# Optimization experiments

Measured on AMD Instinct MI355X. Metric: run time of the kernel, lower is better.

The kernel has to match this reference:

```python
import jax, jax.numpy as jnp
import numpy as np

D_MODEL = 1024
N_HEADS = 16
D_HEAD = D_MODEL // N_HEADS
B, S = 4, 2048


def setup_inputs() -> dict:
    key = jax.random.key(0)
    ks = jax.random.split(key, 12)
    std = 1.0 / np.sqrt(D_MODEL)
    inp = {
        "q": jax.random.normal(ks[0], (B, S, D_MODEL), jnp.float32),
        "k": jax.random.normal(ks[1], (B, S, D_MODEL), jnp.float32),
        "v": jax.random.normal(ks[2], (B, S, D_MODEL), jnp.float32),
        # causal mask: 1 where attention is disallowed (j > i)
        "mask": jnp.triu(jnp.ones((S, S), jnp.int32), k=1)[None, None],
        "Wq": jax.random.normal(ks[3], (D_MODEL, D_MODEL), jnp.float32) * std,
        "bq": jnp.zeros((D_MODEL,), jnp.float32),
        "Wk": jax.random.normal(ks[4], (D_MODEL, D_MODEL), jnp.float32) * std,
        "bk": jnp.zeros((D_MODEL,), jnp.float32),
        "Wv": jax.random.normal(ks[5], (D_MODEL, D_MODEL), jnp.float32) * std,
        "bv": jnp.zeros((D_MODEL,), jnp.float32),
        "Wo": jax.random.normal(ks[6], (D_MODEL, D_MODEL), jnp.float32) * std,
        "bo": jnp.zeros((D_MODEL,), jnp.float32),
    }
    return inp


def _split_heads(x):
    # [B, S, D] -> [B, H, S, d_head]
    b, s, _ = x.shape
    return x.reshape(b, s, N_HEADS, D_HEAD).transpose(0, 2, 1, 3)


def reference(q, k, v, mask, Wq, bq, Wk, bk, Wv, bv, Wo, bo):
    # torch Linear: y = x @ W.T + b
    qh = _split_heads(q @ Wq.T + bq)
    kh = _split_heads(k @ Wk.T + bk)
    vh = _split_heads(v @ Wv.T + bv)
    # NOTE: original scales by sqrt(d_model), not sqrt(d_head)
    scale = 1.0 / np.sqrt(D_MODEL).astype(np.float32)
    logits = jnp.einsum("bhqd,bhkd->bhqk", qh, kh) * scale
    logits = logits + mask.astype(logits.dtype) * (-1e9)
    weights = jax.nn.softmax(logits, axis=-1)
    attn = jnp.einsum("bhqk,bhkd->bhqd", weights, vh)
    attn = attn.transpose(0, 2, 1, 3).reshape(q.shape[0], -1, D_MODEL)
    out = attn @ Wo.T + bo
    return out, weights
```

## Files before the change

### kernel.cpp

```cpp
#include <hip/hip_runtime.h>
#include <stdint.h>

typedef unsigned short u16;
typedef __attribute__((ext_vector_type(8))) short bf16x8;
typedef __attribute__((ext_vector_type(8))) unsigned short us8;
typedef __attribute__((ext_vector_type(4))) float f32x4;

typedef __attribute__((address_space(1))) void as1_void;
typedef __attribute__((address_space(3))) void as3_void;

#define S_LEN 2048
#define DMODEL 1024
#define DH 64
#define NHEADS 16
#define NB 4
#define GM (NB * S_LEN)
#define GN DMODEL
#define GK DMODEL
#define SCALE 0.03125f

__device__ __forceinline__ void gload16(const void* g, void* l) {
  __builtin_amdgcn_global_load_lds((const as1_void*)g, (as3_void*)l, 16, 0, 0);
}
__device__ __forceinline__ float bf2f(u16 u) {
  union { unsigned int i; float f; } x; x.i = ((unsigned int)u) << 16; return x.f;
}
__device__ __forceinline__ u16 f2bf(float f) {
  union { float f; unsigned int i; } x; x.f = f;
  unsigned int u = x.i + 0x7fffu + ((x.i >> 16) & 1u);
  return (u16)(u >> 16);
}
__device__ __forceinline__ f32x4 mfma16(bf16x8 a, bf16x8 b, f32x4 c) {
  return __builtin_amdgcn_mfma_f32_16x16x32_bf16(a, b, c, 0, 0, 0);
}
__device__ __forceinline__ void nt_store4(f32x4 v, float* p) {
  __builtin_nontemporal_store(v, (f32x4*)p);
}

__device__ __forceinline__ void cvt_chunk(const float* s, u16* d, int i) {
  const f32x4 a = *(const f32x4*)(s + (size_t)i * 8);
  const f32x4 b = *(const f32x4*)(s + (size_t)i * 8 + 4);
  us8 o;
  o[0] = f2bf(a[0]); o[1] = f2bf(a[1]); o[2] = f2bf(a[2]); o[3] = f2bf(a[3]);
  o[4] = f2bf(b[0]); o[5] = f2bf(b[1]); o[6] = f2bf(b[2]); o[7] = f2bf(b[3]);
  *(us8*)(d + (size_t)i * 8) = o;
}
__global__ __launch_bounds__(256)
void cvt3(const float* __restrict__ s0, const float* __restrict__ s1,
          const float* __restrict__ s2, u16* __restrict__ d0,
          u16* __restrict__ d1, u16* __restrict__ d2, int n8) {
  const int i = blockIdx.x * 256 + threadIdx.x;
  if (i >= n8) return;
  const float* s; u16* d;
  if (blockIdx.y == 0)      { s = s0; d = d0; }
  else if (blockIdx.y == 1) { s = s1; d = d1; }
  else                      { s = s2; d = d2; }
  cvt_chunk(s, d, i);
}
__global__ __launch_bounds__(256)
void cvt4(const float* __restrict__ s0, const float* __restrict__ s1,
          const float* __restrict__ s2, const float* __restrict__ s3,
          u16* __restrict__ d0, u16* __restrict__ d1,
          u16* __restrict__ d2, u16* __restrict__ d3, int n8) {
  const int i = blockIdx.x * 256 + threadIdx.x;
  if (i >= n8) return;
  const float* s; u16* d;
  if (blockIdx.y == 0)      { s = s0; d = d0; }
  else if (blockIdx.y == 1) { s = s1; d = d1; }
  else if (blockIdx.y == 2) { s = s2; d = d2; }
  else                      { s = s3; d = d3; }
  cvt_chunk(s, d, i);
}

#define GEMM_IDX                                                              \
  const int tid  = threadIdx.x;                                               \
  const int lane = tid & 63;                                                  \
  const int wvi  = tid >> 6;                                                  \
  const int wr   = wvi >> 1, wc = wvi & 1;                                    \
  const int rlow = lane & 15, rhi = lane >> 4;

#define GEMM_COMPUTE(Ab, Bb)                                                  \
  {                                                                           \
    bf16x8 af[4][2], bfr[4][2];                                               \
    _Pragma("unroll")                                                         \
    for (int mi = 0; mi < 4; ++mi) {                                          \
      const int row = wr * 64 + mi * 16 + rlow;                               \
      _Pragma("unroll")                                                       \
      for (int k2 = 0; k2 < 2; ++k2)                                          \
        af[mi][k2] = *(const bf16x8*)&(Ab)[row * 64 +                         \
                     (((rhi + k2 * 4) ^ (row & 7)) << 3)];                    \
    }                                                                         \
    _Pragma("unroll")                                                         \
    for (int ni = 0; ni < 4; ++ni) {                                          \
      const int row = wc * 64 + ni * 16 + rlow;                               \
      _Pragma("unroll")                                                       \
      for (int k2 = 0; k2 < 2; ++k2)                                          \
        bfr[ni][k2] = *(const bf16x8*)&(Bb)[row * 64 +                        \
                      (((rhi + k2 * 4) ^ (row & 7)) << 3)];                   \
    }                                                                         \
    _Pragma("unroll")                                                         \
    for (int mi = 0; mi < 4; ++mi)                                            \
      _Pragma("unroll")                                                       \
      for (int ni = 0; ni < 4; ++ni) {                                        \
        acc[mi][ni] = mfma16(af[mi][0], bfr[ni][0], acc[mi][ni]);             \
        acc[mi][ni] = mfma16(af[mi][1], bfr[ni][1], acc[mi][ni]);             \
      }                                                                       \
  }

__global__ __launch_bounds__(256, 3)
void gemm_qkv(const u16* __restrict__ xq, const u16* __restrict__ xk,
              const u16* __restrict__ xv, const u16* __restrict__ wq,
              const u16* __restrict__ wk, const u16* __restrict__ wv,
              const float* __restrict__ bq, const float* __restrict__ bk,
              const float* __restrict__ bv, u16* __restrict__ oq,
              u16* __restrict__ ok, u16* __restrict__ ov) {
  __shared__ u16 smem[2 * 8192];
  u16* As = smem;
  u16* Bs = smem + 8192;
  const u16 *A, *W; const float* bias; u16* C;
  if (blockIdx.z == 0)      { A = xq; W = wq; bias = bq; C = oq; }
  else if (blockIdx.z == 1) { A = xk; W = wk; bias = bk; C = ok; }
  else                      { A = xv; W = wv; bias = bv; C = ov; }
  GEMM_IDX
  const int m0 = blockIdx.x * 128;
  const int n0 = blockIdx.y * 128;

  f32x4 acc[4][4];
#pragma unroll
  for (int i = 0; i < 4; ++i)
#pragma unroll
    for (int j = 0; j < 4; ++j) acc[i][j] = (f32x4){0.f, 0.f, 0.f, 0.f};

  const int nk = GK >> 6;
  for (int kk = 0; kk < nk; ++kk) {
#pragma unroll
    for (int i = 0; i < 4; ++i) {
      const int c = i * 256 + tid;
      const int row = c >> 3, cw = c & 7;
      const int koff = (kk << 6) + ((cw ^ (row & 7)) << 3);
      gload16(A + (size_t)(m0 + row) * GK + koff, &As[(c - lane) << 3]);
      gload16(W + (size_t)(n0 + row) * GK + koff, &Bs[(c - lane) << 3]);
    }
    __syncthreads();
    GEMM_COMPUTE(As, Bs)
    __syncthreads();
  }

  {
    u16* Cs = smem;
#pragma unroll
    for (int ni = 0; ni < 4; ++ni) {
      const int col = wc * 64 + ni * 16 + rlow;
      const float bv2 = bias[n0 + col];
#pragma unroll
      for (int mi = 0; mi < 4; ++mi)
#pragma unroll
        for (int r = 0; r < 4; ++r)
          Cs[(wr * 64 + mi * 16 + rhi * 4 + r) * 128 + col] = f2bf(acc[mi][ni][r] + bv2);
    }
    __syncthreads();
#pragma unroll
    for (int i = 0; i < 8; ++i) {
      const int c = i * 256 + tid;
      const int row = c >> 4, cw = c & 15;
      const us8 t = *(const us8*)&Cs[row * 128 + cw * 8];
      *(us8*)&C[(size_t)(m0 + row) * GN + n0 + cw * 8] = t;
    }
  }
}

__global__ __launch_bounds__(256, 2)
void gemm_o(const u16* __restrict__ A, const u16* __restrict__ W,
            const float* __restrict__ bias, float* __restrict__ C) {
  __shared__ u16 smem[4 * 8192];
  u16* As = smem;
  u16* Bs = smem + 2 * 8192;
  GEMM_IDX
  const int m0 = blockIdx.x * 128;
  const int n0 = blockIdx.y * 128;

  f32x4 acc[4][4];
#pragma unroll
  for (int i = 0; i < 4; ++i)
#pragma unroll
    for (int j = 0; j < 4; ++j) acc[i][j] = (f32x4){0.f, 0.f, 0.f, 0.f};

#define STAGE_G(bufi, kk)                                                     \
  {                                                                           \
    _Pragma("unroll")                                                         \
    for (int i = 0; i < 4; ++i) {                                             \
      const int c = i * 256 + tid;                                            \
      const int row = c >> 3, cw = c & 7;                                     \
      const int koff = ((kk) << 6) + ((cw ^ (row & 7)) << 3);                 \
      gload16(A + (size_t)(m0 + row) * GK + koff,                             \
              &As[(bufi) * 8192 + ((c - lane) << 3)]);                        \
      gload16(W + (size_t)(n0 + row) * GK + koff,                             \
              &Bs[(bufi) * 8192 + ((c - lane) << 3)]);                        \
    }                                                                         \
  }

  const int nk = GK >> 6;
  STAGE_G(0, 0);
  __syncthreads();
  int buf = 0;
  for (int kk = 0; kk < nk; ++kk) {
    if (kk + 1 < nk) STAGE_G(buf ^ 1, kk + 1);
    const u16* Ab = &As[buf * 8192];
    const u16* Bb = &Bs[buf * 8192];
    GEMM_COMPUTE(Ab, Bb)
    __syncthreads();
    buf ^= 1;
  }
#undef STAGE_G

  {
    float* Cs = (float*)smem;
#pragma unroll
    for (int ni = 0; ni < 4; ++ni) {
      const int col = wc * 64 + ni * 16 + rlow;
      const float bv2 = bias[n0 + col];
#pragma unroll
      for (int mi = 0; mi < 4; ++mi)
#pragma unroll
        for (int r = 0; r < 4; ++r)
          Cs[(wr * 64 + mi * 16 + rhi * 4 + r) * 128 + col] = acc[mi][ni][r] + bv2;
    }
    __syncthreads();
#pragma unroll
    for (int i = 0; i < 16; ++i) {
      const int c = i * 256 + tid;
      const int row = c >> 5, cw = c & 31;
      const f32x4 t = *(const f32x4*)&Cs[row * 128 + cw * 4];
      nt_store4(t, &C[(size_t)(m0 + row) * GN + n0 + cw * 4]);
    }
  }
}

__global__ __launch_bounds__(512, 4)
void attn_fused(const u16* __restrict__ qh, const u16* __restrict__ kh,
                const u16* __restrict__ vh, float* __restrict__ wout,
                u16* __restrict__ am)
{
  __shared__ u16 smem[34304];
  u16* Ws  = smem;
  u16* Qs  = smem;
  u16* Kb1 = smem;
  u16* Kb0 = smem + 17408;
  u16* VT  = smem + 17408 + 8192;

  const int tid = threadIdx.x, lane = tid & 63, wv = tid >> 6;
  const int rlow = lane & 15, rhi = lane >> 4;
  const int idx = blockIdx.x;
  const int bh  = idx & 63;
  const int qt  = 15 - (idx >> 6);
  const int b = bh >> 4, h = bh & 15;
  const int q0 = qt << 7;
  const size_t headoff = (size_t)b * S_LEN * DMODEL + h * DH;

#define STAGE_K(dst, jtile)                                                   \
  {                                                                           \
    _Pragma("unroll")                                                         \
    for (int i = 0; i < 2; ++i) {                                             \
      const int c = i * 512 + tid;                                            \
      const int row = c >> 3, cw = c & 7;                                     \
      gload16(kh + headoff + (size_t)((jtile) * 128 + row) * DMODEL +         \
              ((cw ^ (row & 7)) << 3), &(dst)[(c - lane) << 3]);              \
    }                                                                         \
  }
#define LOAD_V(jtile)                                                         \
  {                                                                           \
    const int d0v = wv << 3;                                                  \
    vvA = *(const bf16x8*)(vh + headoff +                                     \
          (size_t)((jtile) * 128 + lane) * DMODEL + d0v);                     \
    vvB = *(const bf16x8*)(vh + headoff +                                     \
          (size_t)((jtile) * 128 + 64 + lane) * DMODEL + d0v);                \
  }

#pragma unroll
  for (int i = 0; i < 2; ++i) {
    const int c = i * 512 + tid;
    const int row = c >> 3, cw = c & 7;
    gload16(qh + headoff + (size_t)(q0 + row) * DMODEL + ((cw ^ (row & 7)) << 3),
            &Qs[(c - lane) << 3]);
  }
  __syncthreads();
  bf16x8 qf[2];
  {
    const int row = wv * 16 + rlow;
#pragma unroll
    for (int k2 = 0; k2 < 2; ++k2)
      qf[k2] = *(const bf16x8*)&Qs[row * 64 + (((rhi + k2 * 4) ^ (row & 7)) << 3)];
  }

  const int gi_base = q0 + wv * 16 + rhi * 4;
  float ssum[4] = {0.f, 0.f, 0.f, 0.f};

  STAGE_K(Kb0, 0);
  for (int jt = 0; jt <= qt; ++jt) {
    __syncthreads();
    const u16* kcur = (jt & 1) ? Kb1 : Kb0;
    if (jt < qt) {
      u16* knxt = (jt & 1) ? Kb0 : Kb1;
      STAGE_K(knxt, jt + 1);
    }
    const bool diag = (jt == qt);
    float pexp[4] = {0.f, 0.f, 0.f, 0.f};
#pragma unroll
    for (int half = 0; half < 2; ++half) {
      f32x4 acc[4];
#pragma unroll
      for (int ni = 0; ni < 4; ++ni) acc[ni] = (f32x4){0.f, 0.f, 0.f, 0.f};
#pragma unroll
      for (int k2 = 0; k2 < 2; ++k2) {
#pragma unroll
        for (int ni = 0; ni < 4; ++ni) {
          const int row = (half * 4 + ni) * 16 + rlow;
          bf16x8 kf = *(const bf16x8*)&kcur[row * 64 + (((rhi + k2 * 4) ^ (row & 7)) << 3)];
          acc[ni] = mfma16(qf[k2], kf, acc[ni]);
        }
      }
#pragma unroll
      for (int ni = 0; ni < 4; ++ni) {
        const int gj = jt * 128 + (half * 4 + ni) * 16 + rlow;
#pragma unroll
        for (int r = 0; r < 4; ++r) {
          if (!diag || gj <= gi_base + r) pexp[r] += __expf(acc[ni][r] * SCALE);
        }
      }
    }
#pragma unroll
    for (int r = 0; r < 4; ++r) {
      float p = pexp[r];
      p += __shfl_xor(p, 1);
      p += __shfl_xor(p, 2);
      p += __shfl_xor(p, 4);
      p += __shfl_xor(p, 8);
      ssum[r] += p;
    }
  }
  float inv_s[4];
#pragma unroll
  for (int r = 0; r < 4; ++r) inv_s[r] = 1.f / ssum[r];

  f32x4 opv[4];
#pragma unroll
  for (int ni = 0; ni < 4; ++ni) opv[ni] = (f32x4){0.f, 0.f, 0.f, 0.f};

  bf16x8 vvA, vvB;
  __syncthreads();
  STAGE_K(Kb0, 0);
  LOAD_V(0);
  __syncthreads();

  for (int jt = 0; jt <= qt; ++jt) {
    {
      const int d0v = wv << 3;
#pragma unroll
      for (int e = 0; e < 8; ++e) {
        VT[(d0v + e) * 136 + lane] = (u16)vvA[e];
        VT[(d0v + e) * 136 + 64 + lane] = (u16)vvB[e];
      }
    }
    const bool diag = (jt == qt);
#pragma unroll
    for (int half = 0; half < 2; ++half) {
      f32x4 acc[4];
#pragma unroll
      for (int ni = 0; ni < 4; ++ni) acc[ni] = (f32x4){0.f, 0.f, 0.f, 0.f};
#pragma unroll
      for (int k2 = 0; k2 < 2; ++k2) {
#pragma unroll
        for (int ni = 0; ni < 4; ++ni) {
          const int row = (half * 4 + ni) * 16 + rlow;
          bf16x8 kf = *(const bf16x8*)&Kb0[row * 64 + (((rhi + k2 * 4) ^ (row & 7)) << 3)];
          acc[ni] = mfma16(qf[k2], kf, acc[ni]);
        }
      }
#pragma unroll
      for (int ni = 0; ni < 4; ++ni) {
        const int col = (half * 4 + ni) * 16 + rlow;
        const int gj = jt * 128 + col;
#pragma unroll
        for (int r = 0; r < 4; ++r) {
          float w = 0.f;
          if (!diag || gj <= gi_base + r) w = __expf(acc[ni][r] * SCALE) * inv_s[r];
          Ws[(wv * 16 + rhi * 4 + r) * 136 + col] = f2bf(w);
        }
      }
    }
    __syncthreads();
    if (jt < qt) {
      STAGE_K(Kb0, jt + 1);
      LOAD_V(jt + 1);
    }
    {
      const size_t wbase = ((size_t)bh * S_LEN + q0) * S_LEN + (size_t)jt * 128;
#pragma unroll
      for (int i = 0; i < 8; ++i) {
        const int c = i * 512 + tid;
        const int row = c >> 5, cw = c & 31;
        f32x4 t;
        t[0] = bf2f(Ws[row * 136 + cw * 4 + 0]);
        t[1] = bf2f(Ws[row * 136 + cw * 4 + 1]);
        t[2] = bf2f(Ws[row * 136 + cw * 4 + 2]);
        t[3] = bf2f(Ws[row * 136 + cw * 4 + 3]);
        nt_store4(t, wout + wbase + (size_t)row * S_LEN + cw * 4);
      }
    }
#pragma unroll
    for (int k4 = 0; k4 < 4; ++k4) {
      const bf16x8 afr = *(const bf16x8*)&Ws[(wv * 16 + rlow) * 136 + rhi * 8 + k4 * 32];
#pragma unroll
      for (int ni = 0; ni < 4; ++ni) {
        const bf16x8 vfr = *(const bf16x8*)&VT[(ni * 16 + rlow) * 136 + rhi * 8 + k4 * 32];
        opv[ni] = mfma16(afr, vfr, opv[ni]);
      }
    }
    __syncthreads();
  }
#undef STAGE_K
#undef LOAD_V

  {
    const f32x4 z = {0.f, 0.f, 0.f, 0.f};
    for (int jt = qt + 1; jt < 16; ++jt) {
      const size_t wbase = ((size_t)bh * S_LEN + q0) * S_LEN + (size_t)jt * 128;
#pragma unroll
      for (int i = 0; i < 8; ++i) {
        const int c = i * 512 + tid;
        const int row = c >> 5, cw = c & 31;
        nt_store4(z, wout + wbase + (size_t)row * S_LEN + cw * 4);
      }
    }
  }

  {
    u16* Os = smem;
#pragma unroll
    for (int ni = 0; ni < 4; ++ni)
#pragma unroll
      for (int r = 0; r < 4; ++r)
        Os[(wv * 16 + rhi * 4 + r) * 72 + ni * 16 + rlow] = f2bf(opv[ni][r]);
    __syncthreads();
#pragma unroll
    for (int i = 0; i < 2; ++i) {
      const int c = i * 512 + tid;
      const int row = c >> 3, cw = c & 7;
      const us8 t = *(const us8*)&Os[row * 72 + cw * 8];
      *(us8*)(am + headoff + (size_t)(q0 + row) * DMODEL + cw * 8) = t;
    }
  }
}

extern "C" void kernel_launch(void* const* d_in, const int* in_sizes, int n_in,
                              void* d_out, int out_size, void* d_ws, size_t ws_size,
                              hipStream_t stream) {
  const float* q  = (const float*)d_in[0];
  const float* k  = (const float*)d_in[1];
  const float* v  = (const float*)d_in[2];
  const float* Wq = (const float*)d_in[4];
  const float* bq = (const float*)d_in[5];
  const float* Wk = (const float*)d_in[6];
  const float* bk = (const float*)d_in[7];
  const float* Wv = (const float*)d_in[8];
  const float* bv = (const float*)d_in[9];
  const float* Wo = (const float*)d_in[10];
  const float* bo = (const float*)d_in[11];

  const size_t proj_elems = (size_t)NB * S_LEN * DMODEL;
  const size_t w_elems    = (size_t)DMODEL * DMODEL;
  float* out0 = (float*)d_out;
  float* wts  = out0 + proj_elems;

  u16* qh  = (u16*)d_ws;
  u16* kh  = qh + proj_elems;
  u16* vh  = kh + proj_elems;
  u16* am  = vh + proj_elems;
  u16* wco = am + proj_elems;

  u16* xq = (u16*)wts;
  u16* xk = xq + proj_elems;
  u16* xv = xk + proj_elems;
  u16* wq_ = xv + proj_elems;
  u16* wk_ = wq_ + w_elems;
  u16* wv_ = wk_ + w_elems;

  const int n8x = (int)(proj_elems / 8);
  const int n8w = (int)(w_elems / 8);

  cvt3<<<dim3(n8x / 256, 3), dim3(256), 0, stream>>>(q, k, v, xq, xk, xv, n8x);
  cvt4<<<dim3(n8w / 256, 4), dim3(256), 0, stream>>>(Wq, Wk, Wv, Wo,
                                                     wq_, wk_, wv_, wco, n8w);
  gemm_qkv<<<dim3(64, 8, 3), dim3(256), 0, stream>>>(xq, xk, xv, wq_, wk_, wv_,
                                                     bq, bk, bv, qh, kh, vh);
  attn_fused<<<dim3(1024), dim3(512), 0, stream>>>(qh, kh, vh, wts, am);
  gemm_o<<<dim3(64, 8), dim3(256), 0, stream>>>(am, wco, bo, out0);
}
```

Before: 348.3 us.

## Move causal zero-fill of attention weights into the projection GEMM kernels

The upper-triangle zero tiles of the attention weight output are no longer written by the attention kernel. Instead they are spread across the QKV GEMM (heads 3 onward) and the output GEMM (heads 0-2), which gives those compute-bound kernels extra store work and shortens the attention kernel's tail. The bf16 weight copies are moved into the first output buffer so the zero-fill in gemm_qkv does not overwrite staging data it still reads. This relies on careful aliasing of the scratch buffers inside the output tensors.

```diff
diff --git a/kernel.cpp b/kernel.cpp
--- a/kernel.cpp
+++ b/kernel.cpp
@@ -70,6 +70,23 @@
   else if (blockIdx.y == 2) { s = s2; d = d2; }
   else                      { s = s3; d = d3; }
   cvt_chunk(s, d, i);
+}
+
+__device__ __forceinline__ void zero_tiles(float* __restrict__ wz, int tid,
+                                           int zi, int bh_base, int tmax,
+                                           int stride) {
+  const f32x4 z4 = {0.f, 0.f, 0.f, 0.f};
+  for (int t = zi; t < tmax; t += stride) {
+    const int bh = bh_base + t / 120;
+    int r = t % 120;
+    int i = 0;
+    while (r >= 15 - i) { r -= 15 - i; ++i; }
+    const int j = i + 1 + r;
+    float* p = wz + ((size_t)(bh * 2048 + i * 128)) * 2048 + j * 128;
+#pragma unroll 4
+    for (int c = tid; c < 4096; c += 256)
+      nt_store4(z4, p + (size_t)(c >> 5) * 2048 + ((c & 31) << 2));
+  }
 }
 
 #define GEMM_IDX                                                              \
@@ -113,7 +130,8 @@
               const u16* __restrict__ wk, const u16* __restrict__ wv,
               const float* __restrict__ bq, const float* __restrict__ bk,
               const float* __restrict__ bv, u16* __restrict__ oq,
-              u16* __restrict__ ok, u16* __restrict__ ov) {
+              u16* __restrict__ ok, u16* __restrict__ ov,
+              float* __restrict__ wz) {
   __shared__ u16 smem[2 * 8192];
   u16* As = smem;
   u16* Bs = smem + 8192;
@@ -167,11 +185,17 @@
       *(us8*)&C[(size_t)(m0 + row) * GN + n0 + cw * 8] = t;
     }
   }
+
+  {
+    const int fid = blockIdx.x + blockIdx.y * 64 + blockIdx.z * 512;
+    zero_tiles(wz, tid, fid, 3, 7320, 1536);
+  }
 }
 
 __global__ __launch_bounds__(256, 2)
 void gemm_o(const u16* __restrict__ A, const u16* __restrict__ W,
-            const float* __restrict__ bias, float* __restrict__ C) {
+            const float* __restrict__ bias, float* __restrict__ C,
+            float* __restrict__ wz) {
   __shared__ u16 smem[4 * 8192];
   u16* As = smem;
   u16* Bs = smem + 2 * 8192;
@@ -234,6 +258,11 @@
       nt_store4(t, &C[(size_t)(m0 + row) * GN + n0 + cw * 4]);
     }
   }
+
+  {
+    const int fid = blockIdx.x + blockIdx.y * 64;
+    zero_tiles(wz, tid, fid, 0, 360, 512);
+  }
 }
 
 __global__ __launch_bounds__(512, 4)
@@ -420,19 +449,6 @@
   }
 #undef STAGE_K
 #undef LOAD_V
-
-  {
-    const f32x4 z = {0.f, 0.f, 0.f, 0.f};
-    for (int jt = qt + 1; jt < 16; ++jt) {
-      const size_t wbase = ((size_t)bh * S_LEN + q0) * S_LEN + (size_t)jt * 128;
-#pragma unroll
-      for (int i = 0; i < 8; ++i) {
-        const int c = i * 512 + tid;
-        const int row = c >> 5, cw = c & 31;
-        nt_store4(z, wout + wbase + (size_t)row * S_LEN + cw * 4);
-      }
-    }
-  }
 
   {
     u16* Os = smem;
@@ -481,7 +497,7 @@
   u16* xq = (u16*)wts;
   u16* xk = xq + proj_elems;
   u16* xv = xk + proj_elems;
-  u16* wq_ = xv + proj_elems;
+  u16* wq_ = (u16*)out0;
   u16* wk_ = wq_ + w_elems;
   u16* wv_ = wk_ + w_elems;
 
@@ -492,7 +508,7 @@
   cvt4<<<dim3(n8w / 256, 4), dim3(256), 0, stream>>>(Wq, Wk, Wv, Wo,
                                                      wq_, wk_, wv_, wco, n8w);
   gemm_qkv<<<dim3(64, 8, 3), dim3(256), 0, stream>>>(xq, xk, xv, wq_, wk_, wv_,
-                                                     bq, bk, bv, qh, kh, vh);
+                                                     bq, bk, bv, qh, kh, vh, wts);
   attn_fused<<<dim3(1024), dim3(512), 0, stream>>>(qh, kh, vh, wts, am);
-  gemm_o<<<dim3(64, 8), dim3(256), 0, stream>>>(am, wco, bo, out0);
-}
+  gemm_o<<<dim3(64, 8), dim3(256), 0, stream>>>(am, wco, bo, out0, wts);
+}
```

New measurement: 325.4 us. -6.6%, faster.
